# Kernel tuning notes

Measured on AMD Instinct MI355X. Metric: run time of the kernel, lower is better.

The kernel has to match this reference:

```python
import jax, jax.numpy as jnp
import numpy as np

B, C, H, W = 4, 128, 96, 96
INTER = C // 2


def setup_inputs() -> dict:
    key = jax.random.key(0)
    ks = jax.random.split(key, 6)
    scale = 1.0 / np.sqrt(C)
    return {
        "x1": jax.random.normal(ks[0], (B, C, H, W), dtype=jnp.float32),
        "x2": jax.random.normal(ks[1], (B, C, H, W), dtype=jnp.float32),
        "w_theta": jax.random.normal(ks[2], (INTER, C), dtype=jnp.float32) * scale,
        "w_phi": jax.random.normal(ks[3], (INTER, C), dtype=jnp.float32) * scale,
        "w_g": jax.random.normal(ks[4], (INTER, C), dtype=jnp.float32) * scale,
        "w_mask": jax.random.normal(ks[5], (C, INTER), dtype=jnp.float32) * (1.0 / np.sqrt(INTER)),
    }


def reference(x1, x2, w_theta, w_phi, w_g, w_mask):
    b, c, h1, w1 = x1.shape  # c == full channel
    inter = c // 2
    # 1x1 convs (no bias) == channel GEMMs
    theta = jnp.einsum('ic,bchw->bihw', w_theta, x1)   # [b, inter, h1, w1]
    phi   = jnp.einsum('ic,bchw->bihw', w_phi,   x2)   # [b, inter, h2, w2]
    g     = jnp.einsum('ic,bchw->bihw', w_g,     x2)   # [b, inter, h2, w2]
    # Faithful to original: .view(b, c, -1) with c = FULL channel count,
    # so the flattened length is H*W/2 and the contraction dim is c (row-major reshape).
    theta = theta.reshape(b, c, -1).transpose(0, 2, 1)  # [b, N1, c], N1 = h1*w1//2
    phi = phi.reshape(b, c, -1)                         # [b, c, N2]
    g = g.reshape(b, c, -1).transpose(0, 2, 1)          # [b, N2, c]
    scores = jnp.einsum('bnc,bcm->bnm', theta, phi)     # [b, N1, N2]
    attn = jax.nn.softmax(scores, axis=1)               # softmax over dim=1 (query axis!)
    y = jnp.einsum('bnm,bmc->bnc', attn, g)             # [b, N1, c]
    y = y.transpose(0, 2, 1).reshape(b, inter, h1, w1)  # [b, inter, h1, w1]
    mask = jnp.einsum('ci,bihw->bchw', w_mask, y)       # [b, c, h1, w1]
    return mask + x1
```

## Files before the change

kernel.cpp:

```cpp
#include <hip/hip_runtime.h>

typedef __attribute__((ext_vector_type(8))) short short8;
typedef __attribute__((ext_vector_type(4))) float f32x4;
typedef __attribute__((ext_vector_type(16))) float f32x16;
typedef unsigned short u16;
typedef unsigned int u32;

#define NB 4
#define CH 128
#define INTER2 64
#define HW2 9216
#define NN 4608
#define NSLICE 16
#define SLW2 288
#define PCH 136
#define APITCH 136

__device__ __forceinline__ u16 f2bf(float f) {
  u32 u = __float_as_uint(f);
  u += 0x7fffu + ((u >> 16) & 1u);
  return (u16)(u >> 16);
}
__device__ __forceinline__ float bf2f(u16 h) { return __uint_as_float(((u32)h) << 16); }
__device__ __forceinline__ u32 cvtpk(float lo, float hi) {
  u32 r;
  asm("v_cvt_pk_bf16_f32 %0, %1, %2" : "=v"(r) : "v"(lo), "v"(hi));
  return r;
}
__device__ __forceinline__ void gl_lds16(const u16* g, u16* l) {
  __builtin_amdgcn_global_load_lds(
      (const __attribute__((address_space(1))) unsigned int*)g,
      (__attribute__((address_space(3))) unsigned int*)l, 16, 0, 0);
}

__global__ void k_wcvt(const float* __restrict__ wt, const float* __restrict__ wp,
                       const float* __restrict__ wg, const float* __restrict__ wm,
                       u16* __restrict__ wtb, u16* __restrict__ wpb,
                       u16* __restrict__ wgb, u16* __restrict__ wmb) {
  int i = blockIdx.x * 256 + threadIdx.x;
  if (i < CH * INTER2) {
    wtb[i] = f2bf(wt[i]);
    wpb[i] = f2bf(wp[i]);
    wgb[i] = f2bf(wg[i]);
    wmb[i] = f2bf(wm[i]);
  }
}

__global__ __launch_bounds__(256) void k_conv(const float* __restrict__ x1,
                                              const float* __restrict__ x2,
                                              const u16* __restrict__ wtb,
                                              const u16* __restrict__ wpb,
                                              const u16* __restrict__ wgb,
                                              u16* __restrict__ Tt,
                                              u16* __restrict__ Pt,
                                              u16* __restrict__ Gn) {
  __shared__ u16 xT[64 * PCH];
  __shared__ u16 ot[64 * 72];
  const int tid = threadIdx.x;
  const int w = tid >> 6, l = tid & 63, lr = l & 15, lg = l >> 4;
  const int pt = blockIdx.x, b = blockIdx.y, z = blockIdx.z;
  const int p0 = pt * 64;
  const int h = (p0 >= NN) ? 1 : 0;
  const int n0 = p0 - h * NN;
  const float* X = (z ? x2 : x1) + (size_t)b * CH * HW2;

  {
    const int pq = (l & 15) * 4;
    const int cs = w + 4 * (l >> 4);
#pragma unroll
    for (int it = 0; it < 8; it++) {
      const int c = it * 16 + cs;
      float4 v = *(const float4*)(X + (size_t)c * HW2 + p0 + pq);
      xT[(pq + 0) * PCH + c] = f2bf(v.x);
      xT[(pq + 1) * PCH + c] = f2bf(v.y);
      xT[(pq + 2) * PCH + c] = f2bf(v.z);
      xT[(pq + 3) * PCH + c] = f2bf(v.w);
    }
  }
  short8 wsP[4], wsG[4];
  {
    const u16* W1 = z ? wpb : wtb;
#pragma unroll
    for (int ks = 0; ks < 4; ks++)
      wsP[ks] = *(const short8*)(W1 + (w * 16 + lr) * CH + ks * 32 + lg * 8);
    if (z) {
#pragma unroll
      for (int ks = 0; ks < 4; ks++)
        wsG[ks] = *(const short8*)(wgb + (w * 16 + lr) * CH + ks * 32 + lg * 8);
    }
  }
  __syncthreads();
  short8 xf[4][4];
#pragma unroll
  for (int tp = 0; tp < 4; tp++)
#pragma unroll
    for (int ks = 0; ks < 4; ks++)
      xf[tp][ks] = *(const short8*)(&xT[(tp * 16 + lr) * PCH + ks * 32 + lg * 8]);

  f32x4 accP[4];
#pragma unroll
  for (int tp = 0; tp < 4; tp++) {
#pragma unroll
    for (int j = 0; j < 4; j++) accP[tp][j] = 0.f;
#pragma unroll
    for (int ks = 0; ks < 4; ks++)
      accP[tp] = __builtin_amdgcn_mfma_f32_16x16x32_bf16(xf[tp][ks], wsP[ks], accP[tp], 0, 0, 0);
  }
#pragma unroll
  for (int tp = 0; tp < 4; tp++) {
#pragma unroll
    for (int j = 0; j < 4; j++)
      ot[(tp * 16 + lg * 4 + j) * 72 + w * 16 + lr] = f2bf(accP[tp][j]);
  }
  if (z) {
    f32x4 accG[4];
#pragma unroll
    for (int tp = 0; tp < 4; tp++) {
#pragma unroll
      for (int j = 0; j < 4; j++) accG[tp][j] = 0.f;
#pragma unroll
      for (int ks = 0; ks < 4; ks++)
        accG[tp] = __builtin_amdgcn_mfma_f32_16x16x32_bf16(wsG[ks], xf[tp][ks], accG[tp], 0, 0, 0);
    }
    u16* Gb = Gn + (size_t)b * CH * NN;
#pragma unroll
    for (int tp = 0; tp < 4; tp++) {
#pragma unroll
      for (int j = 0; j < 4; j++) {
        const int ig = w * 16 + lg * 4 + j;
        Gb[(size_t)((h << 6) + ig) * NN + n0 + tp * 16 + lr] = f2bf(accG[tp][j]);
      }
    }
  }
  __syncthreads();
  {
    u16* dst = (z ? Pt : Tt) + (size_t)b * NN * CH;
#pragma unroll
    for (int q = 0; q < 2; q++) {
      const int idx = tid * 2 + q;
      const int p = idx >> 3, c8 = (idx & 7) * 8;
      uint4 v = *(const uint4*)(&ot[p * 72 + c8]);
      *(uint4*)(dst + (size_t)(n0 + p) * CH + h * 64 + c8) = v;
    }
  }
}

__global__ __launch_bounds__(256) void k_den(const u16* __restrict__ Tt,
                                             const u16* __restrict__ Pt,
                                             float* __restrict__ denp) {
  const int tid = threadIdx.x;
  const int w = tid >> 6, l = tid & 63, lm = l & 31, lh = l >> 5;
  const int s = blockIdx.x & 15, mt = blockIdx.x >> 4;
  const int b = blockIdx.y;
  const int m0 = mt * 256;
  const int nbase = s * SLW2;
  const u16* PtB = Pt + (size_t)b * NN * CH;
  const u16* TtB = Tt + (size_t)b * NN * CH;

  short8 bf[2][8];
#pragma unroll
  for (int ms = 0; ms < 2; ms++)
#pragma unroll
    for (int ks = 0; ks < 8; ks++)
      bf[ms][ks] = *(const short8*)(PtB + (size_t)(m0 + w * 64 + ms * 32 + lm) * CH + ks * 16 + lh * 8);

  float den0 = 0.f, den1 = 0.f;
  short8 ac[8], an[8];
#pragma unroll
  for (int ks = 0; ks < 8; ks++)
    ac[ks] = *(const short8*)(TtB + (size_t)(nbase + lm) * CH + ks * 16 + lh * 8);

  for (int it = 0; it < 9; it++) {
    if (it + 1 < 9) {
      const int nr = nbase + (it + 1) * 32 + lm;
#pragma unroll
      for (int ks = 0; ks < 8; ks++)
        an[ks] = *(const short8*)(TtB + (size_t)nr * CH + ks * 16 + lh * 8);
    }
    f32x16 a0, a1;
#pragma unroll
    for (int q = 0; q < 16; q++) { a0[q] = 0.f; a1[q] = 0.f; }
#pragma unroll
    for (int ks = 0; ks < 8; ks++) {
      a0 = __builtin_amdgcn_mfma_f32_32x32x16_bf16(ac[ks], bf[0][ks], a0, 0, 0, 0);
      a1 = __builtin_amdgcn_mfma_f32_32x32x16_bf16(ac[ks], bf[1][ks], a1, 0, 0, 0);
    }
#pragma unroll
    for (int q = 0; q < 16; q++) {
      den0 += exp2f(__builtin_fmaf(a0[q], 1.44269504f, -57.70780163f));
      den1 += exp2f(__builtin_fmaf(a1[q], 1.44269504f, -57.70780163f));
    }
    if (it + 1 < 9) {
#pragma unroll
      for (int ks = 0; ks < 8; ks++) ac[ks] = an[ks];
    }
  }
  den0 += __shfl_xor(den0, 32, 64);
  den1 += __shfl_xor(den1, 32, 64);
  if (l < 32) {
    float* dp = denp + (size_t)(s * NB + b) * NN + m0 + w * 64;
    dp[lm] = den0;
    dp[32 + lm] = den1;
  }
}

__global__ __launch_bounds__(256) void k_rdn(const float* __restrict__ denp,
                                             float* __restrict__ rdn) {
  const int i = blockIdx.x * 256 + threadIdx.x;
  const int b = i / NN, m = i % NN;
  float s = 0.f;
#pragma unroll
  for (int s2 = 0; s2 < NSLICE; s2++) s += denp[(size_t)(s2 * NB + b) * NN + m];
  rdn[i] = 1.0f / s;
}

__global__ __launch_bounds__(256) void k_att(const u16* __restrict__ Tt,
                                             const u16* __restrict__ Pt,
                                             const u16* __restrict__ Gn,
                                             const float* __restrict__ rdn,
                                             float* __restrict__ Yp) {
  __shared__ u16 TtS[128 * 128];
  __shared__ u16 Atile[128 * APITCH];
  const int tid = threadIdx.x;
  const int w = tid >> 6, l = tid & 63, lr = l & 15, lg = l >> 4;
  const int lm = l & 31, lh = l >> 5;
  const int x = blockIdx.x;
  const int xcd = x & 7, rr = x >> 3;
  const int nt = rr >> 1;
  const int c = xcd + 8 * (rr & 1);
  const int b = c >> 2, sk = c & 3;
  const int n0 = nt * 128;
  const int mbase = sk * 1152;
  const u16* TtB = Tt + ((size_t)b * NN + n0) * CH;
  const u16* PtB = Pt + (size_t)b * NN * CH;
  const u16* GnB = Gn + (size_t)b * CH * NN;
  const float* rdnB = rdn + b * NN;

#pragma unroll
  for (int it = 0; it < 8; it++) {
    const int i = it * 256 + tid;
    const int row = i >> 4, slot = i & 15;
    gl_lds16(TtB + (size_t)row * CH + ((slot ^ (row & 15)) * 8),
             &TtS[(it * 256 + w * 64) * 8]);
  }
  __syncthreads();

  const int wc = w >> 1, wn = w & 1;
  f32x4 acc[4][4];
#pragma unroll
  for (int fa = 0; fa < 4; fa++)
#pragma unroll
    for (int fb = 0; fb < 4; fb++)
#pragma unroll
      for (int j = 0; j < 4; j++) acc[fa][fb][j] = 0.f;

  for (int ch = 0; ch < 9; ch++) {
    const int mch = mbase + ch * 128;
    short8 bf[8];
#pragma unroll
    for (int ks = 0; ks < 8; ks++)
      bf[ks] = *(const short8*)(PtB + (size_t)(mch + w * 32 + lm) * CH + ks * 16 + lh * 8);
    const float rv = rdnB[mch + w * 32 + lm];
#pragma unroll
    for (int ns = 0; ns < 4; ns++) {
      short8 af[8];
#pragma unroll
      for (int ks = 0; ks < 8; ks++)
        af[ks] = *(const short8*)(&TtS[(ns * 32 + lm) * 128 + (((ks * 2 + lh) ^ (lm & 15)) * 8)]);
      f32x16 sa;
#pragma unroll
      for (int q = 0; q < 16; q++) sa[q] = 0.f;
#pragma unroll
      for (int ks = 0; ks < 8; ks++)
        sa = __builtin_amdgcn_mfma_f32_32x32x16_bf16(af[ks], bf[ks], sa, 0, 0, 0);
#pragma unroll
      for (int q = 0; q < 16; q += 2) {
        const int nl = ns * 32 + (q & 3) + 8 * (q >> 2) + 4 * lh;
        float e0 = exp2f(__builtin_fmaf(sa[q], 1.44269504f, -57.70780163f)) * rv;
        float e1 = exp2f(__builtin_fmaf(sa[q + 1], 1.44269504f, -57.70780163f)) * rv;
        u32 pk = cvtpk(e0, e1);
        Atile[nl * APITCH + w * 32 + lm] = (u16)pk;
        Atile[(nl + 1) * APITCH + w * 32 + lm] = (u16)(pk >> 16);
      }
    }
    __syncthreads();
#pragma unroll
    for (int ks = 0; ks < 4; ks++) {
      short8 gf[4], pb[4];
#pragma unroll
      for (int fa = 0; fa < 4; fa++)
        gf[fa] = *(const short8*)(GnB + (size_t)(wc * 64 + fa * 16 + lr) * NN + mch + ks * 32 + lg * 8);
#pragma unroll
      for (int fb = 0; fb < 4; fb++)
        pb[fb] = *(const short8*)(&Atile[(wn * 64 + fb * 16 + lr) * APITCH + ks * 32 + lg * 8]);
#pragma unroll
      for (int fa = 0; fa < 4; fa++)
#pragma unroll
        for (int fb = 0; fb < 4; fb++)
          acc[fa][fb] = __builtin_amdgcn_mfma_f32_16x16x32_bf16(gf[fa], pb[fb], acc[fa][fb], 0, 0, 0);
    }
    __syncthreads();
  }
  float* Yb = Yp + (size_t)(sk * NB + b) * CH * NN;
#pragma unroll
  for (int fa = 0; fa < 4; fa++) {
#pragma unroll
    for (int fb = 0; fb < 4; fb++) {
      const int n = n0 + wn * 64 + fb * 16 + lr;
#pragma unroll
      for (int j = 0; j < 4; j++) {
        const int d = wc * 64 + fa * 16 + lg * 4 + j;
        Yb[(size_t)d * NN + n] = acc[fa][fb][j];
      }
    }
  }
}

__global__ __launch_bounds__(256) void k_out(const float* __restrict__ Yp,
                                             const u16* __restrict__ wmb,
                                             const float* __restrict__ x1,
                                             float* __restrict__ out) {
  __shared__ u16 yy[64][72];
  const int tid = threadIdx.x;
  const int w = tid >> 6, l = tid & 63, lr = l & 15, lg = l >> 4;
  const int b = blockIdx.y;
  const int n0 = blockIdx.x * 32;
  const int nl = tid & 31, cch = tid >> 5;

  float v[16];
#pragma unroll
  for (int q = 0; q < 16; q++) v[q] = 0.f;
#pragma unroll
  for (int s2 = 0; s2 < 4; s2++) {
    const float* base = Yp + ((size_t)(s2 * NB + b) * CH + cch * 16) * NN + n0 + nl;
#pragma unroll
    for (int q = 0; q < 16; q++) v[q] += base[(size_t)q * NN];
  }
#pragma unroll
  for (int q = 0; q < 16; q++) {
    const int d = cch * 16 + q;
    yy[(d >> 6) * 32 + nl][d & 63] = f2bf(v[q]);
  }
  __syncthreads();

  const int wm3 = w >> 1, wp3 = w & 1;
  f32x4 eacc[4][2];
#pragma unroll
  for (int fa = 0; fa < 4; fa++)
#pragma unroll
    for (int fb = 0; fb < 2; fb++)
#pragma unroll
      for (int j = 0; j < 4; j++) eacc[fa][fb][j] = 0.f;
#pragma unroll
  for (int ks = 0; ks < 2; ks++) {
    short8 wa[4];
#pragma unroll
    for (int fa = 0; fa < 4; fa++)
      wa[fa] = *(const short8*)(wmb + (wm3 * 64 + fa * 16 + lr) * 64 + ks * 32 + lg * 8);
    short8 yb[2];
#pragma unroll
    for (int fb = 0; fb < 2; fb++)
      yb[fb] = *(const short8*)(&yy[wp3 * 32 + fb * 16 + lr][ks * 32 + lg * 8]);
#pragma unroll
    for (int fa = 0; fa < 4; fa++)
#pragma unroll
      for (int fb = 0; fb < 2; fb++)
        eacc[fa][fb] = __builtin_amdgcn_mfma_f32_16x16x32_bf16(wa[fa], yb[fb], eacc[fa][fb], 0, 0, 0);
  }
  const float* x1b = x1 + (size_t)b * CH * HW2;
  float* ob = out + (size_t)b * CH * HW2;
#pragma unroll
  for (int fa = 0; fa < 4; fa++) {
#pragma unroll
    for (int fb = 0; fb < 2; fb++) {
      const int pl = wp3 * 32 + fb * 16 + lr;
      const int col = n0 + (pl & 31) + (pl >> 5) * NN;
#pragma unroll
      for (int j = 0; j < 4; j++) {
        const int c = wm3 * 64 + fa * 16 + lg * 4 + j;
        const size_t o = (size_t)c * HW2 + col;
        ob[o] = eacc[fa][fb][j] + x1b[o];
      }
    }
  }
}

extern "C" void kernel_launch(void* const* d_in, const int* in_sizes, int n_in,
                              void* d_out, int out_size, void* d_ws, size_t ws_size,
                              hipStream_t stream) {
  const float* x1 = (const float*)d_in[0];
  const float* x2 = (const float*)d_in[1];
  const float* wt = (const float*)d_in[2];
  const float* wp = (const float*)d_in[3];
  const float* wg = (const float*)d_in[4];
  const float* wm = (const float*)d_in[5];
  float* out = (float*)d_out;

  char* ws = (char*)d_ws;
  const size_t SZ_T = (size_t)NB * NN * CH * 2;
  u16* Tt = (u16*)ws; ws += SZ_T;
  u16* Pt = (u16*)ws; ws += SZ_T;
  u16* Gn = (u16*)ws; ws += SZ_T;
  float* denp = (float*)ws; ws += (size_t)NSLICE * NB * NN * 4;
  float* rdn = (float*)ws; ws += (size_t)NB * NN * 4;
  u16* wtb = (u16*)ws; ws += (size_t)CH * INTER2 * 2;
  u16* wpb = (u16*)ws; ws += (size_t)CH * INTER2 * 2;
  u16* wgb = (u16*)ws; ws += (size_t)CH * INTER2 * 2;
  u16* wmb = (u16*)ws; ws += (size_t)CH * INTER2 * 2;
  float* Yp = (float*)ws; ws += (size_t)16 * CH * NN * 4;
  if (ws_size < (size_t)(ws - (char*)d_ws)) return;

  hipLaunchKernelGGL(k_wcvt, dim3(32), dim3(256), 0, stream, wt, wp, wg, wm, wtb, wpb, wgb, wmb);
  hipLaunchKernelGGL(k_conv, dim3(144, NB, 2), dim3(256), 0, stream, x1, x2, wtb, wpb, wgb, Tt, Pt, Gn);
  hipLaunchKernelGGL(k_den, dim3(288, NB), dim3(256), 0, stream, Tt, Pt, denp);
  hipLaunchKernelGGL(k_rdn, dim3(72), dim3(256), 0, stream, denp, rdn);
  hipLaunchKernelGGL(k_att, dim3(576), dim3(256), 0, stream, Tt, Pt, Gn, rdn, Yp);
  hipLaunchKernelGGL(k_out, dim3(144, NB), dim3(256), 0, stream, Yp, wmb, x1, out);
}
```

Measured before the change: 198.5 us.

## Prescale G by softmax reciprocal and restructure attention kernel warp tiling

Adds a kernel that multiplies G by the per-key reciprocal denominator ahead of time, so the attention kernel no longer scales each exponential. The attention kernel now keeps each warp's 32 query rows of theta in registers instead of staging a 128x128 theta tile in LDS. The score MFMA is swapped so each warp covers all keys for its own queries, which allows packed 32-bit LDS writes, and the second GEMM is re-split so each warp owns 32 output channels across all 128 queries. It also sets launch bounds with a minimum of 3 blocks and drops the large shared theta buffer to raise occupancy, at the cost of an extra launch, an extra pass over G, and more global P loads per warp.

After: 220.9 us. 1.11x slower.

```diff
diff --git a/kernel.cpp b/kernel.cpp
--- a/kernel.cpp
+++ b/kernel.cpp
@@ -214,12 +214,36 @@
   rdn[i] = 1.0f / s;
 }
 
-__global__ __launch_bounds__(256) void k_att(const u16* __restrict__ Tt,
-                                             const u16* __restrict__ Pt,
-                                             const u16* __restrict__ Gn,
-                                             const float* __restrict__ rdn,
-                                             float* __restrict__ Yp) {
-  __shared__ u16 TtS[128 * 128];
+__global__ __launch_bounds__(256) void k_gd(const u16* __restrict__ Gn,
+                                            const float* __restrict__ rdn,
+                                            u16* __restrict__ Gd) {
+  const int q = blockIdx.x * 256 + threadIdx.x;
+  const int d = q / 576, mc = q % 576;
+  const int m0 = mc * 8;
+  const int b = blockIdx.y;
+  const float* rp = rdn + (size_t)b * NN + m0;
+  float4 r0 = *(const float4*)rp;
+  float4 r1 = *(const float4*)(rp + 4);
+  float rr[8] = {r0.x, r0.y, r0.z, r0.w, r1.x, r1.y, r1.z, r1.w};
+  const size_t off = (size_t)b * CH * NN + (size_t)d * NN + m0;
+  uint4 v = *(const uint4*)(Gn + off);
+  u32 arr[4] = {v.x, v.y, v.z, v.w};
+  uint4 o;
+  u32 ov[4];
+#pragma unroll
+  for (int j = 0; j < 4; j++) {
+    float lo = bf2f((u16)(arr[j] & 0xffffu)) * rr[2 * j];
+    float hi = bf2f((u16)(arr[j] >> 16)) * rr[2 * j + 1];
+    ov[j] = cvtpk(lo, hi);
+  }
+  o.x = ov[0]; o.y = ov[1]; o.z = ov[2]; o.w = ov[3];
+  *(uint4*)(Gd + off) = o;
+}
+
+__global__ __launch_bounds__(256, 3) void k_att(const u16* __restrict__ Tt,
+                                                const u16* __restrict__ Pt,
+                                                const u16* __restrict__ Gd,
+                                                float* __restrict__ Yp) {
   __shared__ u16 Atile[128 * APITCH];
   const int tid = threadIdx.x;
   const int w = tid >> 6, l = tid & 63, lr = l & 15, lg = l >> 4;
@@ -231,85 +255,73 @@
   const int b = c >> 2, sk = c & 3;
   const int n0 = nt * 128;
   const int mbase = sk * 1152;
-  const u16* TtB = Tt + ((size_t)b * NN + n0) * CH;
+  const u16* TtB = Tt + (size_t)b * NN * CH;
   const u16* PtB = Pt + (size_t)b * NN * CH;
-  const u16* GnB = Gn + (size_t)b * CH * NN;
-  const float* rdnB = rdn + b * NN;
-
-#pragma unroll
-  for (int it = 0; it < 8; it++) {
-    const int i = it * 256 + tid;
-    const int row = i >> 4, slot = i & 15;
-    gl_lds16(TtB + (size_t)row * CH + ((slot ^ (row & 15)) * 8),
-             &TtS[(it * 256 + w * 64) * 8]);
-  }
-  __syncthreads();
-
-  const int wc = w >> 1, wn = w & 1;
-  f32x4 acc[4][4];
-#pragma unroll
-  for (int fa = 0; fa < 4; fa++)
-#pragma unroll
-    for (int fb = 0; fb < 4; fb++)
+  const u16* GdB = Gd + (size_t)b * CH * NN;
+
+  short8 af[8];
+#pragma unroll
+  for (int ks = 0; ks < 8; ks++)
+    af[ks] = *(const short8*)(TtB + (size_t)(n0 + w * 32 + lm) * CH + ks * 16 + lh * 8);
+
+  f32x4 acc[2][8];
+#pragma unroll
+  for (int fa = 0; fa < 2; fa++)
+#pragma unroll
+    for (int fb = 0; fb < 8; fb++)
 #pragma unroll
       for (int j = 0; j < 4; j++) acc[fa][fb][j] = 0.f;
 
   for (int ch = 0; ch < 9; ch++) {
     const int mch = mbase + ch * 128;
-    short8 bf[8];
-#pragma unroll
-    for (int ks = 0; ks < 8; ks++)
-      bf[ks] = *(const short8*)(PtB + (size_t)(mch + w * 32 + lm) * CH + ks * 16 + lh * 8);
-    const float rv = rdnB[mch + w * 32 + lm];
-#pragma unroll
-    for (int ns = 0; ns < 4; ns++) {
-      short8 af[8];
+#pragma unroll
+    for (int ms = 0; ms < 4; ms++) {
+      short8 bfm[8];
 #pragma unroll
       for (int ks = 0; ks < 8; ks++)
-        af[ks] = *(const short8*)(&TtS[(ns * 32 + lm) * 128 + (((ks * 2 + lh) ^ (lm & 15)) * 8)]);
+        bfm[ks] = *(const short8*)(PtB + (size_t)(mch + ms * 32 + lm) * CH + ks * 16 + lh * 8);
       f32x16 sa;
 #pragma unroll
       for (int q = 0; q < 16; q++) sa[q] = 0.f;
 #pragma unroll
       for (int ks = 0; ks < 8; ks++)
-        sa = __builtin_amdgcn_mfma_f32_32x32x16_bf16(af[ks], bf[ks], sa, 0, 0, 0);
-#pragma unroll
-      for (int q = 0; q < 16; q += 2) {
-        const int nl = ns * 32 + (q & 3) + 8 * (q >> 2) + 4 * lh;
-        float e0 = exp2f(__builtin_fmaf(sa[q], 1.44269504f, -57.70780163f)) * rv;
-        float e1 = exp2f(__builtin_fmaf(sa[q + 1], 1.44269504f, -57.70780163f)) * rv;
+        sa = __builtin_amdgcn_mfma_f32_32x32x16_bf16(bfm[ks], af[ks], sa, 0, 0, 0);
+#pragma unroll
+      for (int t = 0; t < 8; t++) {
+        float e0 = exp2f(__builtin_fmaf(sa[2 * t], 1.44269504f, -57.70780163f));
+        float e1 = exp2f(__builtin_fmaf(sa[2 * t + 1], 1.44269504f, -57.70780163f));
         u32 pk = cvtpk(e0, e1);
-        Atile[nl * APITCH + w * 32 + lm] = (u16)pk;
-        Atile[(nl + 1) * APITCH + w * 32 + lm] = (u16)(pk >> 16);
+        const int mloc = ms * 32 + ((2 * t) & 3) + 8 * ((2 * t) >> 2) + 4 * lh;
+        *(u32*)(&Atile[(w * 32 + lm) * APITCH + mloc]) = pk;
       }
     }
     __syncthreads();
 #pragma unroll
     for (int ks = 0; ks < 4; ks++) {
-      short8 gf[4], pb[4];
-#pragma unroll
-      for (int fa = 0; fa < 4; fa++)
-        gf[fa] = *(const short8*)(GnB + (size_t)(wc * 64 + fa * 16 + lr) * NN + mch + ks * 32 + lg * 8);
-#pragma unroll
-      for (int fb = 0; fb < 4; fb++)
-        pb[fb] = *(const short8*)(&Atile[(wn * 64 + fb * 16 + lr) * APITCH + ks * 32 + lg * 8]);
-#pragma unroll
-      for (int fa = 0; fa < 4; fa++)
-#pragma unroll
-        for (int fb = 0; fb < 4; fb++)
+      short8 gf[2], pb[8];
+#pragma unroll
+      for (int fa = 0; fa < 2; fa++)
+        gf[fa] = *(const short8*)(GdB + (size_t)(w * 32 + fa * 16 + lr) * NN + mch + ks * 32 + lg * 8);
+#pragma unroll
+      for (int fb = 0; fb < 8; fb++)
+        pb[fb] = *(const short8*)(&Atile[(fb * 16 + lr) * APITCH + ks * 32 + lg * 8]);
+#pragma unroll
+      for (int fa = 0; fa < 2; fa++)
+#pragma unroll
+        for (int fb = 0; fb < 8; fb++)
           acc[fa][fb] = __builtin_amdgcn_mfma_f32_16x16x32_bf16(gf[fa], pb[fb], acc[fa][fb], 0, 0, 0);
     }
     __syncthreads();
   }
   float* Yb = Yp + (size_t)(sk * NB + b) * CH * NN;
 #pragma unroll
-  for (int fa = 0; fa < 4; fa++) {
-#pragma unroll
-    for (int fb = 0; fb < 4; fb++) {
-      const int n = n0 + wn * 64 + fb * 16 + lr;
+  for (int fa = 0; fa < 2; fa++) {
+#pragma unroll
+    for (int fb = 0; fb < 8; fb++) {
+      const int n = n0 + fb * 16 + lr;
 #pragma unroll
       for (int j = 0; j < 4; j++) {
-        const int d = wc * 64 + fa * 16 + lg * 4 + j;
+        const int d = w * 32 + fa * 16 + lg * 4 + j;
         Yb[(size_t)d * NN + n] = acc[fa][fb][j];
       }
     }
@@ -401,6 +413,7 @@
   u16* Tt = (u16*)ws; ws += SZ_T;
   u16* Pt = (u16*)ws; ws += SZ_T;
   u16* Gn = (u16*)ws; ws += SZ_T;
+  u16* Gd = (u16*)ws; ws += SZ_T;
   float* denp = (float*)ws; ws += (size_t)NSLICE * NB * NN * 4;
   float* rdn = (float*)ws; ws += (size_t)NB * NN * 4;
   u16* wtb = (u16*)ws; ws += (size_t)CH * INTER2 * 2;
@@ -414,6 +427,7 @@
   hipLaunchKernelGGL(k_conv, dim3(144, NB, 2), dim3(256), 0, stream, x1, x2, wtb, wpb, wgb, Tt, Pt, Gn);
   hipLaunchKernelGGL(k_den, dim3(288, NB), dim3(256), 0, stream, Tt, Pt, denp);
   hipLaunchKernelGGL(k_rdn, dim3(72), dim3(256), 0, stream, denp, rdn);
-  hipLaunchKernelGGL(k_att, dim3(576), dim3(256), 0, stream, Tt, Pt, Gn, rdn, Yp);
+  hipLaunchKernelGGL(k_gd, dim3(288, NB), dim3(256), 0, stream, Gn, rdn, Gd);
+  hipLaunchKernelGGL(k_att, dim3(576), dim3(256), 0, stream, Tt, Pt, Gd, Yp);
   hipLaunchKernelGGL(k_out, dim3(144, NB), dim3(256), 0, stream, Yp, wmb, x1, out);
 }
```
